# Optimization experiments

Hardware: AMD Instinct MI355X
Metric: run time of the kernel (lower is better)

Reference implementation:

```python
import jax, jax.numpy as jnp
import numpy as np

A_DIM = 12      # action dim (half of augmented state)
N_STEPS = 10    # Heun ODE steps (Flow.N)
P = 0.95        # mixing coefficient in _Heun_method


def _mlp(x, obs, t, W1, b1, W2, b2, W3, b3, W4, b4):
    h = jnp.concatenate([x, obs, t], axis=-1)
    h = jnp.tanh(h @ W1 + b1)
    h = jnp.tanh(h @ W2 + b2)
    h = jnp.tanh(h @ W3 + b3)
    return h @ W4 + b4


def _heun(obs, x, params):
    # Flow._Heun_method: sequential Heun integration of the augmented state.
    z = x[..., :A_DIM]
    y = x[..., A_DIM:]
    dt = 1.0 / N_STEPS
    tshape = x.shape[:-1] + (1,)

    def step(carry, i):
        z, y = carry
        t = jnp.ones(tshape, x.dtype) * (i / N_STEPS)
        z_t = _mlp(y, obs, t, *params)
        z_in = z + z_t * dt
        y_t = _mlp(z_in, obs, t, *params)
        y_in = y + y_t * dt
        z_new = P * z_in + (1.0 - P) * y_in
        y_new = P * y_in + (1.0 - P) * z_new
        return (z_new, y_new), None

    (z, y), _ = jax.lax.scan(step, (z, y), jnp.arange(N_STEPS, dtype=x.dtype))
    return jnp.concatenate([z, y], axis=-1)


def setup_inputs() -> dict:
    key = jax.random.key(0)
    ks = jax.random.split(key, 8)
    B, OBS, H, A = 2048, 48, 256, A_DIM
    din = A + OBS + 1  # 61
    s = 0.05  # small init scale to keep tanh unsaturated
    return {
        "observations": jax.random.normal(ks[0], (B, OBS), jnp.float32),
        "action_aug_0": jax.random.normal(ks[1], (B, 2 * A), jnp.float32),
        "W1": s * jax.random.normal(ks[2], (din, H), jnp.float32),
        "b1": jnp.zeros((H,), jnp.float32),
        "W2": s * jax.random.normal(ks[3], (H, H), jnp.float32),
        "b2": jnp.zeros((H,), jnp.float32),
        "W3": s * jax.random.normal(ks[4], (H, H), jnp.float32),
        "b3": jnp.zeros((H,), jnp.float32),
        "W4": s * jax.random.normal(ks[5], (H, A), jnp.float32),
        "b4": jnp.zeros((A,), jnp.float32),
        "jac": 1,
    }


def reference(observations, action_aug_0, W1, b1, W2, b2, W3, b3, W4, b4, jac):
    params = (W1, b1, W2, b2, W3, b3, W4, b4)
    action_aug = _heun(observations, action_aug_0, params)
    d = action_aug_0.shape[-1]
    # Normal(0, I) log prob summed over dims
    log_probs = -0.5 * jnp.sum(action_aug_0 ** 2, axis=-1) - 0.5 * d * jnp.log(2.0 * jnp.pi)
    if jac:
        single = lambda o, x: _heun(o, x, params)  # per-sample (obs_dim,), (2a,)
        J = jax.vmap(jax.jacrev(single, argnums=1))(observations, action_aug_0)  # (B, 2a, 2a)
        _, logabsdet = jnp.linalg.slogdet(J)  # = log|det J|
        log_probs = log_probs - logabsdet
    return action_aug, log_probs
```

## Files before the change

### kernel.cpp

```cpp
#include <hip/hip_runtime.h>
#include <hip/hip_bf16.h>


typedef unsigned short ushort_t;
typedef float f32x4 __attribute__((ext_vector_type(4)));
typedef short s16x8 __attribute__((ext_vector_type(8)));

#define NB      2048
#define OBS_D   48
#define XDIM    24
#define NSTEPS  10
#define DT      0.1f
#define PP      0.95f
#define SCL     2.885390081777927f

#define W1U  0
#define W2U  16384
#define W3U  81920
#define W4U  147456
#define W1AU 151552
#define FRAG_BLOCKS 624
#define LP_BLOCKS 8

#define LDS_BUFA 0
#define LDS_BUFB 8192
#define LDS_AIN  16384
#define LDS_PART 17408
#define LDS_TOTAL 25600

__device__ __forceinline__ ushort_t f2bf(float f) {
  unsigned u = __builtin_bit_cast(unsigned, f);
  u += 0x7fffu + ((u >> 16) & 1u);
  return (ushort_t)(u >> 16);
}

__device__ __forceinline__ float tanh_s(float u) {
  float e = __builtin_amdgcn_exp2f(u);
  return __builtin_fmaf(-2.f, __builtin_amdgcn_rcpf(1.f + e), 1.f);
}

__device__ __forceinline__ int pair_byte(int c) {
  return (((c >> 5) << 6) | ((c & 15) << 2) | (((c >> 4) & 1) << 1));
}

__global__ void prep_kernel(const float* __restrict__ W1, const float* __restrict__ b1,
                            const float* __restrict__ W2, const float* __restrict__ W3,
                            const float* __restrict__ W4, const float* __restrict__ x0,
                            const int* __restrict__ jac, float* __restrict__ out,
                            ushort_t* __restrict__ ws) {
  int bid = blockIdx.x;
  int tid = threadIdx.x;
  if (bid < FRAG_BLOCKS) {
    int e = bid * 256 + tid;
    float val = 0.f;
    if (e < 16384) {
      int kt = e >> 13; int r = e & 8191;
      int nt = r >> 9, l = (r >> 3) & 63, j = r & 7;
      int k = kt * 32 + ((l >> 4) << 2) + (j >> 1) + ((j & 1) << 4);
      int col = nt * 16 + (l & 15);
      val = SCL * ((k < 61) ? W1[k * 256 + col] : ((k == 61) ? b1[col] : 0.f));
    } else if (e < 81920) {
      int e2 = e - 16384;
      int kt = e2 >> 13; int r = e2 & 8191;
      int nt = r >> 9, l = (r >> 3) & 63, j = r & 7;
      int k = kt * 32 + ((l >> 4) << 2) + (j >> 1) + ((j & 1) << 4);
      val = SCL * W2[k * 256 + nt * 16 + (l & 15)];
    } else if (e < 147456) {
      int e2 = e - 81920;
      int kt = e2 >> 13; int r = e2 & 8191;
      int nt = r >> 9, l = (r >> 3) & 63, j = r & 7;
      int k = kt * 32 + ((l >> 4) << 2) + (j >> 1) + ((j & 1) << 4);
      val = SCL * W3[k * 256 + nt * 16 + (l & 15)];
    } else if (e < 151552) {
      int e2 = e - 147456;
      int kt = e2 >> 9; int r = e2 & 511;
      int l = (r >> 3) & 63, j = r & 7;
      int k = kt * 32 + ((l >> 4) << 2) + (j >> 1) + ((j & 1) << 4);
      int col = l & 15;
      val = (col < 12) ? W4[k * 12 + col] : 0.f;
    } else {
      int e2 = e - 151552;
      int nt = e2 >> 9; int r = e2 & 511;
      int l = (r >> 3) & 63, j = r & 7;
      int k = ((l >> 4) << 2) + (j >> 1) + ((j & 1) << 4);
      val = (k < 12) ? SCL * W1[k * 256 + nt * 16 + (l & 15)] : 0.f;
    }
    ws[e] = f2bf(val);
  } else {
    int s = (bid - FRAG_BLOCKS) * 256 + tid;
    float acc = 0.f;
    #pragma unroll 4
    for (int j = 0; j < XDIM; ++j) { float v = x0[s * XDIM + j]; acc += v * v; }
    float C = (jac[0] != 0) ? -9.744134143900015f : -22.054524796912143f;
    out[NB * XDIM + s] = -0.5f * acc + C;
  }
}

__global__ __launch_bounds__(512, 2) void flow_main(
    const float* __restrict__ obs, const float* __restrict__ x0,
    const float* __restrict__ W1g, const float* __restrict__ b2g,
    const float* __restrict__ b3g, const float* __restrict__ b4g,
    const ushort_t* __restrict__ ws, float* __restrict__ out) {
  __shared__ char lds[LDS_TOTAL];
  const int tid  = threadIdx.x;
  const int lane = tid & 63;
  const int wv   = tid >> 6;
  const int g    = lane >> 4;
  const int ar   = lane & 15;
  const int row0 = blockIdx.x * 16;
  const int sw   = (ar & 7) << 4;
  const int rs   = tid >> 4, cs = tid & 15;

  ((unsigned*)(lds + LDS_BUFB))[tid] = 0u;
  if (tid < 256) ((unsigned*)(lds + LDS_AIN))[tid] = 0u;
  __syncthreads();

  for (int idx = tid; idx < 16 * OBS_D; idx += 512) {
    int r = idx / OBS_D, o = idx - r * OBS_D;
    int byt = pair_byte(12 + o) ^ ((r & 7) << 4);
    *(ushort_t*)(lds + LDS_BUFB + r * 128 + byt) = f2bf(obs[(row0 + r) * OBS_D + o]);
  }
  if (tid < 16)
    *(ushort_t*)(lds + LDS_BUFB + tid * 128 + (pair_byte(61) ^ ((tid & 7) << 4))) = (ushort_t)0x3F80;

  float zr = 0.f, yr = 0.f, zir = 0.f;
  if (tid < 256 && cs < 12) {
    zr = x0[(row0 + rs) * XDIM + cs];
    yr = x0[(row0 + rs) * XDIM + 12 + cs];
    *(ushort_t*)(lds + LDS_AIN + rs * 64 + ((cs * 4) ^ ((rs & 3) << 4))) = f2bf(yr);
  }

  s16x8 w1o[2][2];
  s16x8 w1a[2], w2r[8][2], w3r[8][2], w4r;
  #pragma unroll
  for (int kt = 0; kt < 2; ++kt)
    #pragma unroll
    for (int n = 0; n < 2; ++n)
      w1o[kt][n] = *(const s16x8*)(ws + W1U + (((kt * 16) + (2 * wv + n)) * 64 + lane) * 8);
  #pragma unroll
  for (int n = 0; n < 2; ++n)
    w1a[n] = *(const s16x8*)(ws + W1AU + (((2 * wv + n)) * 64 + lane) * 8);
  #pragma unroll
  for (int kt = 0; kt < 8; ++kt)
    #pragma unroll
    for (int n = 0; n < 2; ++n) {
      w2r[kt][n] = *(const s16x8*)(ws + W2U + (((kt * 16) + (2 * wv + n)) * 64 + lane) * 8);
      w3r[kt][n] = *(const s16x8*)(ws + W3U + (((kt * 16) + (2 * wv + n)) * 64 + lane) * 8);
    }
  w4r = *(const s16x8*)(ws + W4U + (wv * 64 + lane) * 8);
  asm volatile("" : "+v"(w1a[0]), "+v"(w1a[1]), "+v"(w4r));
  #pragma unroll
  for (int kt = 0; kt < 8; ++kt)
    asm volatile("" : "+v"(w2r[kt][0]), "+v"(w2r[kt][1]), "+v"(w3r[kt][0]), "+v"(w3r[kt][1]));

  const float w1t0 = SCL * W1g[60 * 256 + 32 * wv + ar];
  const float w1t1 = SCL * W1g[60 * 256 + 32 * wv + 16 + ar];
  const float b2s0 = SCL * b2g[32 * wv + ar],      b2s1 = SCL * b2g[32 * wv + 16 + ar];
  const float b3s0 = SCL * b3g[32 * wv + ar],      b3s1 = SCL * b3g[32 * wv + 16 + ar];
  const float b4v  = (cs < 12) ? b4g[cs] : 0.f;

  __syncthreads();

  const f32x4 z4 = {0.f, 0.f, 0.f, 0.f};
  f32x4 ci0 = z4, ci1 = z4;
  #pragma unroll
  for (int kt = 0; kt < 2; ++kt) {
    s16x8 a = *(const s16x8*)(lds + LDS_BUFB + ar * 128 + ((kt * 64 + g * 16) ^ sw));
    ci0 = __builtin_amdgcn_mfma_f32_16x16x32_bf16(a, w1o[kt][0], ci0, 0, 0, 0);
    ci1 = __builtin_amdgcn_mfma_f32_16x16x32_bf16(a, w1o[kt][1], ci1, 0, 0, 0);
  }

  for (int i = 0; i < NSTEPS; ++i) {
    const float t = (float)i * DT;
    const float t0 = __builtin_fmaf(t, w1t0, 0.f), t1 = __builtin_fmaf(t, w1t1, 0.f);
    #pragma unroll
    for (int ev = 0; ev < 2; ++ev) {
      f32x4 acc0 = ci0, acc1 = ci1;
      #pragma unroll
      for (int r = 0; r < 4; ++r) { acc0[r] += t0; acc1[r] += t1; }
      {
        s16x8 a = *(const s16x8*)(lds + LDS_AIN + ar * 64 + ((g * 16) ^ ((ar & 3) << 4)));
        acc0 = __builtin_amdgcn_mfma_f32_16x16x32_bf16(a, w1a[0], acc0, 0, 0, 0);
        acc1 = __builtin_amdgcn_mfma_f32_16x16x32_bf16(a, w1a[1], acc1, 0, 0, 0);
      }
      #pragma unroll
      for (int r = 0; r < 4; ++r) {
        int rw = g * 4 + r;
        float lo = tanh_s(acc0[r]), hi = tanh_s(acc1[r]);
        unsigned p;
        asm("v_cvt_pk_bf16_f32 %0, %1, %2" : "=v"(p) : "v"(lo), "v"(hi));
        *(unsigned*)(lds + LDS_BUFA + rw * 512 + ((wv * 64 + ar * 4) ^ ((rw & 7) << 4))) = p;
      }
      __syncthreads();

      f32x4 a0a = {b2s0, b2s0, b2s0, b2s0}, a1a = {b2s1, b2s1, b2s1, b2s1};
      f32x4 a0b = z4, a1b = z4;
      #pragma unroll
      for (int kt = 0; kt < 4; ++kt) {
        s16x8 a = *(const s16x8*)(lds + LDS_BUFA + ar * 512 + ((kt * 64 + g * 16) ^ sw));
        s16x8 b = *(const s16x8*)(lds + LDS_BUFA + ar * 512 + (((kt + 4) * 64 + g * 16) ^ sw));
        a0a = __builtin_amdgcn_mfma_f32_16x16x32_bf16(a, w2r[kt][0], a0a, 0, 0, 0);
        a1a = __builtin_amdgcn_mfma_f32_16x16x32_bf16(a, w2r[kt][1], a1a, 0, 0, 0);
        a0b = __builtin_amdgcn_mfma_f32_16x16x32_bf16(b, w2r[kt + 4][0], a0b, 0, 0, 0);
        a1b = __builtin_amdgcn_mfma_f32_16x16x32_bf16(b, w2r[kt + 4][1], a1b, 0, 0, 0);
      }
      acc0 = a0a + a0b; acc1 = a1a + a1b;
      #pragma unroll
      for (int r = 0; r < 4; ++r) {
        int rw = g * 4 + r;
        float lo = tanh_s(acc0[r]), hi = tanh_s(acc1[r]);
        unsigned p;
        asm("v_cvt_pk_bf16_f32 %0, %1, %2" : "=v"(p) : "v"(lo), "v"(hi));
        *(unsigned*)(lds + LDS_BUFB + rw * 512 + ((wv * 64 + ar * 4) ^ ((rw & 7) << 4))) = p;
      }
      __syncthreads();

      a0a = (f32x4){b3s0, b3s0, b3s0, b3s0}; a1a = (f32x4){b3s1, b3s1, b3s1, b3s1};
      a0b = z4; a1b = z4;
      #pragma unroll
      for (int kt = 0; kt < 4; ++kt) {
        s16x8 a = *(const s16x8*)(lds + LDS_BUFB + ar * 512 + ((kt * 64 + g * 16) ^ sw));
        s16x8 b = *(const s16x8*)(lds + LDS_BUFB + ar * 512 + (((kt + 4) * 64 + g * 16) ^ sw));
        a0a = __builtin_amdgcn_mfma_f32_16x16x32_bf16(a, w3r[kt][0], a0a, 0, 0, 0);
        a1a = __builtin_amdgcn_mfma_f32_16x16x32_bf16(a, w3r[kt][1], a1a, 0, 0, 0);
        a0b = __builtin_amdgcn_mfma_f32_16x16x32_bf16(b, w3r[kt + 4][0], a0b, 0, 0, 0);
        a1b = __builtin_amdgcn_mfma_f32_16x16x32_bf16(b, w3r[kt + 4][1], a1b, 0, 0, 0);
      }
      acc0 = a0a + a0b; acc1 = a1a + a1b;
      #pragma unroll
      for (int r = 0; r < 4; ++r) {
        int rw = g * 4 + r;
        float lo = tanh_s(acc0[r]), hi = tanh_s(acc1[r]);
        unsigned p;
        asm("v_cvt_pk_bf16_f32 %0, %1, %2" : "=v"(p) : "v"(lo), "v"(hi));
        *(unsigned*)(lds + LDS_BUFA + rw * 512 + ((wv * 64 + ar * 4) ^ ((rw & 7) << 4))) = p;
      }

      asm volatile("s_waitcnt lgkmcnt(0)" ::: "memory");
      __builtin_amdgcn_sched_barrier(0);
      {
        s16x8 a = *(const s16x8*)(lds + LDS_BUFA + ar * 512 + ((wv * 64 + g * 16) ^ sw));
        f32x4 p4 = __builtin_amdgcn_mfma_f32_16x16x32_bf16(a, w4r, z4, 0, 0, 0);
        #pragma unroll
        for (int r = 0; r < 4; ++r)
          *(float*)(lds + LDS_PART + (((g * 4 + r) * 128 + ar * 8 + wv) << 2)) = p4[r];
      }
      __syncthreads();

      if (tid < 256) {
        const char* pb = lds + LDS_PART + ((rs * 128 + cs * 8) << 2);
        f32x4 va = *(const f32x4*)pb;
        f32x4 vb = *(const f32x4*)(pb + 16);
        f32x4 sv = va + vb;
        float s = ((sv[0] + sv[1]) + (sv[2] + sv[3])) + b4v;
        if (cs < 12) {
          int byt = rs * 64 + ((cs * 4) ^ ((rs & 3) << 4));
          if (ev == 0) {
            zir = zr + DT * s;
            *(ushort_t*)(lds + LDS_AIN + byt) = f2bf(zir);
          } else {
            float yi = yr + DT * s;
            zr = PP * zir + (1.f - PP) * yi;
            yr = PP * yi + (1.f - PP) * zr;
            *(ushort_t*)(lds + LDS_AIN + byt) = f2bf(yr);
          }
        }
      }
      __syncthreads();
    }
  }

  if (tid < 256 && cs < 12) {
    out[(row0 + rs) * XDIM + cs]      = zr;
    out[(row0 + rs) * XDIM + 12 + cs] = yr;
  }
}

extern "C" void kernel_launch(void* const* d_in, const int* in_sizes, int n_in,
                              void* d_out, int out_size, void* d_ws, size_t ws_size,
                              hipStream_t stream) {
  const float* obs = (const float*)d_in[0];
  const float* x0  = (const float*)d_in[1];
  const float* W1  = (const float*)d_in[2];
  const float* b1  = (const float*)d_in[3];
  const float* W2  = (const float*)d_in[4];
  const float* b2  = (const float*)d_in[5];
  const float* W3  = (const float*)d_in[6];
  const float* b3  = (const float*)d_in[7];
  const float* W4  = (const float*)d_in[8];
  const float* b4  = (const float*)d_in[9];
  const int*   jac = (const int*)d_in[10];
  float* out = (float*)d_out;
  ushort_t* ws = (ushort_t*)d_ws;

  prep_kernel<<<FRAG_BLOCKS + LP_BLOCKS, 256, 0, stream>>>(W1, b1, W2, W3, W4, x0, jac, out, ws);
  flow_main<<<128, 512, 0, stream>>>(obs, x0, W1, b2, b3, b4, ws, out);
}
```

Baseline: 48.55 us.

## Compute output layer redundantly per wave to drop cross-wave reduction barriers

Each wave now computes the full final layer (W4) over all K tiles itself, so the partial-sum LDS exchange and the extra block barrier per evaluation go away. Triple-buffered hidden activations let one barrier per layer suffice. The state update is kept in MFMA accumulator layout and moved into the A-fragment through a per-wave LDS transpose. The time input is folded into the augmented W1 fragment instead of being added separately. The cost is redundant W4 MFMAs in every wave, more registers for the full W4 fragments, and more LDS.

```diff
diff --git a/kernel.cpp b/kernel.cpp
--- a/kernel.cpp
+++ b/kernel.cpp
@@ -22,11 +22,12 @@
 #define FRAG_BLOCKS 624
 #define LP_BLOCKS 8
 
-#define LDS_BUFA 0
-#define LDS_BUFB 8192
-#define LDS_AIN  16384
-#define LDS_PART 17408
-#define LDS_TOTAL 25600
+#define LDS_B0   0
+#define LDS_B1   8192
+#define LDS_B2   16384
+#define LDS_SCR  24576
+#define LDS_STG  34816
+#define LDS_TOTAL 36864
 
 __device__ __forceinline__ ushort_t f2bf(float f) {
   unsigned u = __builtin_bit_cast(unsigned, f);
@@ -83,7 +84,9 @@
       int nt = e2 >> 9; int r = e2 & 511;
       int l = (r >> 3) & 63, j = r & 7;
       int k = ((l >> 4) << 2) + (j >> 1) + ((j & 1) << 4);
-      val = (k < 12) ? SCL * W1[k * 256 + nt * 16 + (l & 15)] : 0.f;
+      int col = nt * 16 + (l & 15);
+      val = (k < 12) ? SCL * W1[k * 256 + col]
+          : ((k == 16) ? SCL * W1[60 * 256 + col] : 0.f);
     }
     ws[e] = f2bf(val);
   } else {
@@ -98,9 +101,9 @@
 
 __global__ __launch_bounds__(512, 2) void flow_main(
     const float* __restrict__ obs, const float* __restrict__ x0,
-    const float* __restrict__ W1g, const float* __restrict__ b2g,
-    const float* __restrict__ b3g, const float* __restrict__ b4g,
-    const ushort_t* __restrict__ ws, float* __restrict__ out) {
+    const float* __restrict__ b2g, const float* __restrict__ b3g,
+    const float* __restrict__ b4g, const ushort_t* __restrict__ ws,
+    float* __restrict__ out) {
   __shared__ char lds[LDS_TOTAL];
   const int tid  = threadIdx.x;
   const int lane = tid & 63;
@@ -109,29 +112,50 @@
   const int ar   = lane & 15;
   const int row0 = blockIdx.x * 16;
   const int sw   = (ar & 7) << 4;
-  const int rs   = tid >> 4, cs = tid & 15;
-
-  ((unsigned*)(lds + LDS_BUFB))[tid] = 0u;
-  if (tid < 256) ((unsigned*)(lds + LDS_AIN))[tid] = 0u;
+
+  int roff[8], woff[4], swoff[4];
+  #pragma unroll
+  for (int kt = 0; kt < 8; ++kt) roff[kt] = ar * 512 + ((kt * 64 + g * 16) ^ sw);
+  #pragma unroll
+  for (int r = 0; r < 4; ++r) {
+    int rw = 4 * g + r;
+    woff[r]  = rw * 512 + ((wv * 64 + ar * 4) ^ ((rw & 7) << 4));
+    swoff[r] = LDS_SCR + wv * 1280 + rw * 80 + ar * 4;
+  }
+  const int sroff = LDS_SCR + wv * 1280 + ar * 80 + g * 16;
+
+  ((unsigned*)(lds + LDS_STG))[tid] = 0u;
   __syncthreads();
-
   for (int idx = tid; idx < 16 * OBS_D; idx += 512) {
     int r = idx / OBS_D, o = idx - r * OBS_D;
     int byt = pair_byte(12 + o) ^ ((r & 7) << 4);
-    *(ushort_t*)(lds + LDS_BUFB + r * 128 + byt) = f2bf(obs[(row0 + r) * OBS_D + o]);
+    *(ushort_t*)(lds + LDS_STG + r * 128 + byt) = f2bf(obs[(row0 + r) * OBS_D + o]);
   }
   if (tid < 16)
-    *(ushort_t*)(lds + LDS_BUFB + tid * 128 + (pair_byte(61) ^ ((tid & 7) << 4))) = (ushort_t)0x3F80;
-
-  float zr = 0.f, yr = 0.f, zir = 0.f;
-  if (tid < 256 && cs < 12) {
-    zr = x0[(row0 + rs) * XDIM + cs];
-    yr = x0[(row0 + rs) * XDIM + 12 + cs];
-    *(ushort_t*)(lds + LDS_AIN + rs * 64 + ((cs * 4) ^ ((rs & 3) << 4))) = f2bf(yr);
-  }
-
-  s16x8 w1o[2][2];
-  s16x8 w1a[2], w2r[8][2], w3r[8][2], w4r;
+    *(ushort_t*)(lds + LDS_STG + tid * 128 + (pair_byte(61) ^ ((tid & 7) << 4))) = (ushort_t)0x3F80;
+
+  float zst[4], yst[4], zin[4];
+  #pragma unroll
+  for (int r = 0; r < 4; ++r) {
+    int row = row0 + 4 * g + r;
+    zst[r] = (ar < 12) ? x0[row * XDIM + ar] : 0.f;
+    yst[r] = (ar < 12) ? x0[row * XDIM + 12 + ar] : 0.f;
+    zin[r] = 0.f;
+  }
+
+  union FU { s16x8 v; unsigned u[4]; };
+  FU af;
+  {
+    f32x4 av = {0.f, 0.f, 0.f, 0.f};
+    if (g < 3) av = *(const f32x4*)(x0 + (row0 + ar) * XDIM + 12 + 4 * g);
+    const float zf = 0.f;
+    asm("v_cvt_pk_bf16_f32 %0, %1, %2" : "=v"(af.u[0]) : "v"(av[0]), "v"(zf));
+    asm("v_cvt_pk_bf16_f32 %0, %1, %2" : "=v"(af.u[1]) : "v"(av[1]), "v"(zf));
+    asm("v_cvt_pk_bf16_f32 %0, %1, %2" : "=v"(af.u[2]) : "v"(av[2]), "v"(zf));
+    asm("v_cvt_pk_bf16_f32 %0, %1, %2" : "=v"(af.u[3]) : "v"(av[3]), "v"(zf));
+  }
+
+  s16x8 w1o[2][2], w1a[2], w2r[8][2], w3r[8][2], w4F[8];
   #pragma unroll
   for (int kt = 0; kt < 2; ++kt)
     #pragma unroll
@@ -139,25 +163,25 @@
       w1o[kt][n] = *(const s16x8*)(ws + W1U + (((kt * 16) + (2 * wv + n)) * 64 + lane) * 8);
   #pragma unroll
   for (int n = 0; n < 2; ++n)
-    w1a[n] = *(const s16x8*)(ws + W1AU + (((2 * wv + n)) * 64 + lane) * 8);
-  #pragma unroll
-  for (int kt = 0; kt < 8; ++kt)
+    w1a[n] = *(const s16x8*)(ws + W1AU + ((2 * wv + n) * 64 + lane) * 8);
+  #pragma unroll
+  for (int kt = 0; kt < 8; ++kt) {
     #pragma unroll
     for (int n = 0; n < 2; ++n) {
       w2r[kt][n] = *(const s16x8*)(ws + W2U + (((kt * 16) + (2 * wv + n)) * 64 + lane) * 8);
       w3r[kt][n] = *(const s16x8*)(ws + W3U + (((kt * 16) + (2 * wv + n)) * 64 + lane) * 8);
     }
-  w4r = *(const s16x8*)(ws + W4U + (wv * 64 + lane) * 8);
-  asm volatile("" : "+v"(w1a[0]), "+v"(w1a[1]), "+v"(w4r));
+    w4F[kt] = *(const s16x8*)(ws + W4U + (kt * 64 + lane) * 8);
+  }
+  asm volatile("" : "+v"(w1a[0]), "+v"(w1a[1]));
   #pragma unroll
   for (int kt = 0; kt < 8; ++kt)
-    asm volatile("" : "+v"(w2r[kt][0]), "+v"(w2r[kt][1]), "+v"(w3r[kt][0]), "+v"(w3r[kt][1]));
-
-  const float w1t0 = SCL * W1g[60 * 256 + 32 * wv + ar];
-  const float w1t1 = SCL * W1g[60 * 256 + 32 * wv + 16 + ar];
-  const float b2s0 = SCL * b2g[32 * wv + ar],      b2s1 = SCL * b2g[32 * wv + 16 + ar];
-  const float b3s0 = SCL * b3g[32 * wv + ar],      b3s1 = SCL * b3g[32 * wv + 16 + ar];
-  const float b4v  = (cs < 12) ? b4g[cs] : 0.f;
+    asm volatile("" : "+v"(w2r[kt][0]), "+v"(w2r[kt][1]), "+v"(w3r[kt][0]),
+                     "+v"(w3r[kt][1]), "+v"(w4F[kt]));
+
+  const float b2s0 = SCL * b2g[32 * wv + ar],  b2s1 = SCL * b2g[32 * wv + 16 + ar];
+  const float b3s0 = SCL * b3g[32 * wv + ar],  b3s1 = SCL * b3g[32 * wv + 16 + ar];
+  const float b4s  = (ar < 12) ? b4g[ar] : 0.f;
 
   __syncthreads();
 
@@ -165,114 +189,112 @@
   f32x4 ci0 = z4, ci1 = z4;
   #pragma unroll
   for (int kt = 0; kt < 2; ++kt) {
-    s16x8 a = *(const s16x8*)(lds + LDS_BUFB + ar * 128 + ((kt * 64 + g * 16) ^ sw));
+    s16x8 a = *(const s16x8*)(lds + LDS_STG + ar * 128 + ((kt * 64 + g * 16) ^ sw));
     ci0 = __builtin_amdgcn_mfma_f32_16x16x32_bf16(a, w1o[kt][0], ci0, 0, 0, 0);
     ci1 = __builtin_amdgcn_mfma_f32_16x16x32_bf16(a, w1o[kt][1], ci1, 0, 0, 0);
   }
 
+  auto EVAL = [&](f32x4& p4) {
+    f32x4 acc0 = ci0, acc1 = ci1;
+    acc0 = __builtin_amdgcn_mfma_f32_16x16x32_bf16(af.v, w1a[0], acc0, 0, 0, 0);
+    acc1 = __builtin_amdgcn_mfma_f32_16x16x32_bf16(af.v, w1a[1], acc1, 0, 0, 0);
+    #pragma unroll
+    for (int r = 0; r < 4; ++r) {
+      unsigned p;
+      float lo = tanh_s(acc0[r]), hi = tanh_s(acc1[r]);
+      asm("v_cvt_pk_bf16_f32 %0, %1, %2" : "=v"(p) : "v"(lo), "v"(hi));
+      *(unsigned*)(lds + LDS_B0 + woff[r]) = p;
+    }
+    __syncthreads();
+    f32x4 a0a = {b2s0, b2s0, b2s0, b2s0}, a1a = {b2s1, b2s1, b2s1, b2s1};
+    f32x4 a0b = z4, a1b = z4;
+    #pragma unroll
+    for (int kt = 0; kt < 4; ++kt) {
+      s16x8 a = *(const s16x8*)(lds + LDS_B0 + roff[kt]);
+      s16x8 b = *(const s16x8*)(lds + LDS_B0 + roff[kt + 4]);
+      a0a = __builtin_amdgcn_mfma_f32_16x16x32_bf16(a, w2r[kt][0], a0a, 0, 0, 0);
+      a1a = __builtin_amdgcn_mfma_f32_16x16x32_bf16(a, w2r[kt][1], a1a, 0, 0, 0);
+      a0b = __builtin_amdgcn_mfma_f32_16x16x32_bf16(b, w2r[kt + 4][0], a0b, 0, 0, 0);
+      a1b = __builtin_amdgcn_mfma_f32_16x16x32_bf16(b, w2r[kt + 4][1], a1b, 0, 0, 0);
+    }
+    acc0 = a0a + a0b; acc1 = a1a + a1b;
+    #pragma unroll
+    for (int r = 0; r < 4; ++r) {
+      unsigned p;
+      float lo = tanh_s(acc0[r]), hi = tanh_s(acc1[r]);
+      asm("v_cvt_pk_bf16_f32 %0, %1, %2" : "=v"(p) : "v"(lo), "v"(hi));
+      *(unsigned*)(lds + LDS_B1 + woff[r]) = p;
+    }
+    __syncthreads();
+    a0a = (f32x4){b3s0, b3s0, b3s0, b3s0}; a1a = (f32x4){b3s1, b3s1, b3s1, b3s1};
+    a0b = z4; a1b = z4;
+    #pragma unroll
+    for (int kt = 0; kt < 4; ++kt) {
+      s16x8 a = *(const s16x8*)(lds + LDS_B1 + roff[kt]);
+      s16x8 b = *(const s16x8*)(lds + LDS_B1 + roff[kt + 4]);
+      a0a = __builtin_amdgcn_mfma_f32_16x16x32_bf16(a, w3r[kt][0], a0a, 0, 0, 0);
+      a1a = __builtin_amdgcn_mfma_f32_16x16x32_bf16(a, w3r[kt][1], a1a, 0, 0, 0);
+      a0b = __builtin_amdgcn_mfma_f32_16x16x32_bf16(b, w3r[kt + 4][0], a0b, 0, 0, 0);
+      a1b = __builtin_amdgcn_mfma_f32_16x16x32_bf16(b, w3r[kt + 4][1], a1b, 0, 0, 0);
+    }
+    acc0 = a0a + a0b; acc1 = a1a + a1b;
+    #pragma unroll
+    for (int r = 0; r < 4; ++r) {
+      unsigned p;
+      float lo = tanh_s(acc0[r]), hi = tanh_s(acc1[r]);
+      asm("v_cvt_pk_bf16_f32 %0, %1, %2" : "=v"(p) : "v"(lo), "v"(hi));
+      *(unsigned*)(lds + LDS_B2 + woff[r]) = p;
+    }
+    __syncthreads();
+    f32x4 pa = {b4s, b4s, b4s, b4s}, pb = z4;
+    #pragma unroll
+    for (int kt = 0; kt < 4; ++kt) {
+      s16x8 a = *(const s16x8*)(lds + LDS_B2 + roff[kt]);
+      s16x8 b = *(const s16x8*)(lds + LDS_B2 + roff[kt + 4]);
+      pa = __builtin_amdgcn_mfma_f32_16x16x32_bf16(a, w4F[kt], pa, 0, 0, 0);
+      pb = __builtin_amdgcn_mfma_f32_16x16x32_bf16(b, w4F[kt + 4], pb, 0, 0, 0);
+    }
+    p4 = pa + pb;
+  };
+
+  auto TRANSPOSE = [&](const float* val, float tnext) {
+    #pragma unroll
+    for (int r = 0; r < 4; ++r)
+      *(float*)(lds + swoff[r]) = (ar < 12) ? val[r] : 0.f;
+    asm volatile("s_waitcnt lgkmcnt(0)" ::: "memory");
+    __builtin_amdgcn_sched_barrier(0);
+    f32x4 a4 = *(const f32x4*)(lds + sroff);
+    float hi0 = (g == 0) ? tnext : 0.f;
+    const float zf = 0.f;
+    asm("v_cvt_pk_bf16_f32 %0, %1, %2" : "=v"(af.u[0]) : "v"(a4[0]), "v"(hi0));
+    asm("v_cvt_pk_bf16_f32 %0, %1, %2" : "=v"(af.u[1]) : "v"(a4[1]), "v"(zf));
+    asm("v_cvt_pk_bf16_f32 %0, %1, %2" : "=v"(af.u[2]) : "v"(a4[2]), "v"(zf));
+    asm("v_cvt_pk_bf16_f32 %0, %1, %2" : "=v"(af.u[3]) : "v"(a4[3]), "v"(zf));
+  };
+
   for (int i = 0; i < NSTEPS; ++i) {
-    const float t = (float)i * DT;
-    const float t0 = __builtin_fmaf(t, w1t0, 0.f), t1 = __builtin_fmaf(t, w1t1, 0.f);
-    #pragma unroll
-    for (int ev = 0; ev < 2; ++ev) {
-      f32x4 acc0 = ci0, acc1 = ci1;
-      #pragma unroll
-      for (int r = 0; r < 4; ++r) { acc0[r] += t0; acc1[r] += t1; }
-      {
-        s16x8 a = *(const s16x8*)(lds + LDS_AIN + ar * 64 + ((g * 16) ^ ((ar & 3) << 4)));
-        acc0 = __builtin_amdgcn_mfma_f32_16x16x32_bf16(a, w1a[0], acc0, 0, 0, 0);
-        acc1 = __builtin_amdgcn_mfma_f32_16x16x32_bf16(a, w1a[1], acc1, 0, 0, 0);
-      }
-      #pragma unroll
-      for (int r = 0; r < 4; ++r) {
-        int rw = g * 4 + r;
-        float lo = tanh_s(acc0[r]), hi = tanh_s(acc1[r]);
-        unsigned p;
-        asm("v_cvt_pk_bf16_f32 %0, %1, %2" : "=v"(p) : "v"(lo), "v"(hi));
-        *(unsigned*)(lds + LDS_BUFA + rw * 512 + ((wv * 64 + ar * 4) ^ ((rw & 7) << 4))) = p;
-      }
-      __syncthreads();
-
-      f32x4 a0a = {b2s0, b2s0, b2s0, b2s0}, a1a = {b2s1, b2s1, b2s1, b2s1};
-      f32x4 a0b = z4, a1b = z4;
-      #pragma unroll
-      for (int kt = 0; kt < 4; ++kt) {
-        s16x8 a = *(const s16x8*)(lds + LDS_BUFA + ar * 512 + ((kt * 64 + g * 16) ^ sw));
-        s16x8 b = *(const s16x8*)(lds + LDS_BUFA + ar * 512 + (((kt + 4) * 64 + g * 16) ^ sw));
-        a0a = __builtin_amdgcn_mfma_f32_16x16x32_bf16(a, w2r[kt][0], a0a, 0, 0, 0);
-        a1a = __builtin_amdgcn_mfma_f32_16x16x32_bf16(a, w2r[kt][1], a1a, 0, 0, 0);
-        a0b = __builtin_amdgcn_mfma_f32_16x16x32_bf16(b, w2r[kt + 4][0], a0b, 0, 0, 0);
-        a1b = __builtin_amdgcn_mfma_f32_16x16x32_bf16(b, w2r[kt + 4][1], a1b, 0, 0, 0);
-      }
-      acc0 = a0a + a0b; acc1 = a1a + a1b;
-      #pragma unroll
-      for (int r = 0; r < 4; ++r) {
-        int rw = g * 4 + r;
-        float lo = tanh_s(acc0[r]), hi = tanh_s(acc1[r]);
-        unsigned p;
-        asm("v_cvt_pk_bf16_f32 %0, %1, %2" : "=v"(p) : "v"(lo), "v"(hi));
-        *(unsigned*)(lds + LDS_BUFB + rw * 512 + ((wv * 64 + ar * 4) ^ ((rw & 7) << 4))) = p;
-      }
-      __syncthreads();
-
-      a0a = (f32x4){b3s0, b3s0, b3s0, b3s0}; a1a = (f32x4){b3s1, b3s1, b3s1, b3s1};
-      a0b = z4; a1b = z4;
-      #pragma unroll
-      for (int kt = 0; kt < 4; ++kt) {
-        s16x8 a = *(const s16x8*)(lds + LDS_BUFB + ar * 512 + ((kt * 64 + g * 16) ^ sw));
-        s16x8 b = *(const s16x8*)(lds + LDS_BUFB + ar * 512 + (((kt + 4) * 64 + g * 16) ^ sw));
-        a0a = __builtin_amdgcn_mfma_f32_16x16x32_bf16(a, w3r[kt][0], a0a, 0, 0, 0);
-        a1a = __builtin_amdgcn_mfma_f32_16x16x32_bf16(a, w3r[kt][1], a1a, 0, 0, 0);
-        a0b = __builtin_amdgcn_mfma_f32_16x16x32_bf16(b, w3r[kt + 4][0], a0b, 0, 0, 0);
-        a1b = __builtin_amdgcn_mfma_f32_16x16x32_bf16(b, w3r[kt + 4][1], a1b, 0, 0, 0);
-      }
-      acc0 = a0a + a0b; acc1 = a1a + a1b;
-      #pragma unroll
-      for (int r = 0; r < 4; ++r) {
-        int rw = g * 4 + r;
-        float lo = tanh_s(acc0[r]), hi = tanh_s(acc1[r]);
-        unsigned p;
-        asm("v_cvt_pk_bf16_f32 %0, %1, %2" : "=v"(p) : "v"(lo), "v"(hi));
-        *(unsigned*)(lds + LDS_BUFA + rw * 512 + ((wv * 64 + ar * 4) ^ ((rw & 7) << 4))) = p;
-      }
-
-      asm volatile("s_waitcnt lgkmcnt(0)" ::: "memory");
-      __builtin_amdgcn_sched_barrier(0);
-      {
-        s16x8 a = *(const s16x8*)(lds + LDS_BUFA + ar * 512 + ((wv * 64 + g * 16) ^ sw));
-        f32x4 p4 = __builtin_amdgcn_mfma_f32_16x16x32_bf16(a, w4r, z4, 0, 0, 0);
-        #pragma unroll
-        for (int r = 0; r < 4; ++r)
-          *(float*)(lds + LDS_PART + (((g * 4 + r) * 128 + ar * 8 + wv) << 2)) = p4[r];
-      }
-      __syncthreads();
-
-      if (tid < 256) {
-        const char* pb = lds + LDS_PART + ((rs * 128 + cs * 8) << 2);
-        f32x4 va = *(const f32x4*)pb;
-        f32x4 vb = *(const f32x4*)(pb + 16);
-        f32x4 sv = va + vb;
-        float s = ((sv[0] + sv[1]) + (sv[2] + sv[3])) + b4v;
-        if (cs < 12) {
-          int byt = rs * 64 + ((cs * 4) ^ ((rs & 3) << 4));
-          if (ev == 0) {
-            zir = zr + DT * s;
-            *(ushort_t*)(lds + LDS_AIN + byt) = f2bf(zir);
-          } else {
-            float yi = yr + DT * s;
-            zr = PP * zir + (1.f - PP) * yi;
-            yr = PP * yi + (1.f - PP) * zr;
-            *(ushort_t*)(lds + LDS_AIN + byt) = f2bf(yr);
-          }
-        }
-      }
-      __syncthreads();
-    }
-  }
-
-  if (tid < 256 && cs < 12) {
-    out[(row0 + rs) * XDIM + cs]      = zr;
-    out[(row0 + rs) * XDIM + 12 + cs] = yr;
+    f32x4 p4;
+    EVAL(p4);
+    #pragma unroll
+    for (int r = 0; r < 4; ++r) zin[r] = __builtin_fmaf(DT, p4[r], zst[r]);
+    TRANSPOSE(zin, (float)i * DT);
+    EVAL(p4);
+    #pragma unroll
+    for (int r = 0; r < 4; ++r) {
+      float yi = __builtin_fmaf(DT, p4[r], yst[r]);
+      zst[r] = PP * zin[r] + (1.f - PP) * yi;
+      yst[r] = PP * yi + (1.f - PP) * zst[r];
+    }
+    TRANSPOSE(yst, (float)(i + 1) * DT);
+  }
+
+  if (wv == 0 && ar < 12) {
+    #pragma unroll
+    for (int r = 0; r < 4; ++r) {
+      int row = row0 + 4 * g + r;
+      out[row * XDIM + ar]      = zst[r];
+      out[row * XDIM + 12 + ar] = yst[r];
+    }
   }
 }
 
@@ -294,5 +316,5 @@
   ushort_t* ws = (ushort_t*)d_ws;
 
   prep_kernel<<<FRAG_BLOCKS + LP_BLOCKS, 256, 0, stream>>>(W1, b1, W2, W3, W4, x0, jac, out, ws);
-  flow_main<<<128, 512, 0, stream>>>(obs, x0, W1, b2, b3, b4, ws, out);
-}
+  flow_main<<<128, 512, 0, stream>>>(obs, x0, b2, b3, b4, ws, out);
+}
```

Measured after the change: 49.37 us. Within noise of the previous version (+1.7%).
